# Performance work log

Hardware: AMD Instinct MI355X
Metric: run time of the kernel (lower is better)

The kernel has to match this reference:

```python
import jax, jax.numpy as jnp
import numpy as np


def _maxpool2x2(x):
    # x: [B, C, H, W] -> [B, C, H//2, W//2], 2x2 max pool stride 2
    B, C, H, W = x.shape
    return x.reshape(B, C, H // 2, 2, W // 2, 2).max(axis=(3, 5))


def setup_inputs() -> dict:
    key = jax.random.key(0)
    ks = jax.random.split(key, 5)
    C = 64
    B, H, W = 16, 64, 64
    x = jax.random.normal(ks[0], (B, C, H, W), dtype=jnp.float32)
    s = 0.05
    W_theta = jax.random.normal(ks[1], (C // 8, C), dtype=jnp.float32) * s
    W_phi = jax.random.normal(ks[2], (C // 8, C), dtype=jnp.float32) * s
    W_g = jax.random.normal(ks[3], (C // 2, C), dtype=jnp.float32) * s
    W_attn = jax.random.normal(ks[4], (C, C // 2), dtype=jnp.float32) * s
    sigma = jnp.zeros((1,), dtype=jnp.float32)
    return {"x": x, "W_theta": W_theta, "W_phi": W_phi, "W_g": W_g,
            "W_attn": W_attn, "sigma": sigma}


def reference(x, W_theta, W_phi, W_g, W_attn, sigma):
    B, C, H, W = x.shape
    HW = H * W
    # 1x1 convs are channel GEMMs
    theta = jnp.einsum('oc,bchw->bohw', W_theta, x).reshape(B, C // 8, HW)
    phi = jnp.einsum('oc,bchw->bohw', W_phi, x)
    phi = _maxpool2x2(phi).reshape(B, C // 8, HW // 4)
    # attn: [B, HW, HW//4]
    attn = jax.nn.softmax(jnp.einsum('bcq,bck->bqk', theta, phi), axis=-1)
    g = jnp.einsum('oc,bchw->bohw', W_g, x)
    g = _maxpool2x2(g).reshape(B, C // 2, HW // 4)
    # attn_g: [B, C//2, HW]
    attn_g = jnp.einsum('bck,bqk->bcq', g, attn).reshape(B, C // 2, H, W)
    attn_g = jnp.einsum('oc,bchw->bohw', W_attn, attn_g)
    return x + sigma[0] * attn_g
```

## Files before the change

### kernel.cpp

```cpp
#include <hip/hip_runtime.h>
#include <math.h>

#define B_ 16
#define C_ 64
#define HW_ 4096
#define PHW_ 1024

typedef __attribute__((ext_vector_type(8))) short bf8;
typedef __attribute__((ext_vector_type(16))) float fv16;

union FU { bf8 v; unsigned u[4]; };

__device__ inline unsigned short f2bf(float f) {
    unsigned u = __float_as_uint(f);
    return (unsigned short)((u + 0x7FFFu + ((u >> 16) & 1u)) >> 16);
}
__device__ inline unsigned packbf(float a, float b) {
    return (unsigned)f2bf(a) | ((unsigned)f2bf(b) << 16);
}
__device__ inline unsigned packtr(float a, float b) {
    return (__float_as_uint(a) >> 16) | (__float_as_uint(b) & 0xFFFF0000u);
}

__global__ __launch_bounds__(256) void conv_stage(
    const float* __restrict__ x,
    const float* __restrict__ Wt,
    const float* __restrict__ Wp,
    const float* __restrict__ Wg,
    float* __restrict__ theta,
    unsigned short* __restrict__ phi_pack,
    unsigned short* __restrict__ g_pack)
{
    __shared__ float sx[64][128];
    __shared__ float poolh[2][40][33];

    const int t  = threadIdx.x;
    const int b  = blockIdx.x >> 5;
    const int h2 = blockIdx.x & 31;

    const float* xbase = x + (size_t)b * C_ * HW_ + h2 * 128;
    for (int f = t; f < 2048; f += 256) {
        int c = f >> 5, j4 = f & 31;
        *(float4*)&sx[c][j4 * 4] = *(const float4*)&xbase[(size_t)c * HW_ + j4 * 4];
    }

    const int wv = t >> 6, lane = t & 63, lo = lane & 31, hi = lane >> 5;

    FU wa[2][4];
    {
        const float* r0 = (lo < 8)  ? (Wt + lo * 64)
                        : (lo < 16) ? (Wp + (lo - 8) * 64)
                                    : (Wg + (lo - 16) * 64);
        const float* r1 = Wg + ((lo < 16) ? (16 + lo) : 0) * 64;
#pragma unroll
        for (int cs = 0; cs < 4; cs++) {
            const int c0 = cs * 16 + hi * 8;
            float4 a0 = *(const float4*)&r0[c0];
            float4 b0 = *(const float4*)&r0[c0 + 4];
            wa[0][cs].u[0] = packbf(a0.x, a0.y); wa[0][cs].u[1] = packbf(a0.z, a0.w);
            wa[0][cs].u[2] = packbf(b0.x, b0.y); wa[0][cs].u[3] = packbf(b0.z, b0.w);
            float4 a1 = *(const float4*)&r1[c0];
            float4 b1 = *(const float4*)&r1[c0 + 4];
            if (lo >= 16) { a1 = make_float4(0.f,0.f,0.f,0.f); b1 = make_float4(0.f,0.f,0.f,0.f); }
            wa[1][cs].u[0] = packbf(a1.x, a1.y); wa[1][cs].u[1] = packbf(a1.z, a1.w);
            wa[1][cs].u[2] = packbf(b1.x, b1.y); wa[1][cs].u[3] = packbf(b1.z, b1.w);
        }
    }
    __syncthreads();

    fv16 acc0, acc1;
#pragma unroll
    for (int r = 0; r < 16; r++) { acc0[r] = 0.f; acc1[r] = 0.f; }

    const int px = wv * 32 + lo;
#pragma unroll
    for (int cs = 0; cs < 4; cs++) {
        const float* sp = &sx[cs * 16 + hi * 8][px];
        float v[8];
#pragma unroll
        for (int j = 0; j < 8; j++) v[j] = sp[j * 128];
        FU xb;
        xb.u[0] = packbf(v[0], v[1]); xb.u[1] = packbf(v[2], v[3]);
        xb.u[2] = packbf(v[4], v[5]); xb.u[3] = packbf(v[6], v[7]);
        acc0 = __builtin_amdgcn_mfma_f32_32x32x16_bf16(wa[0][cs].v, xb.v, acc0, 0, 0, 0);
        acc1 = __builtin_amdgcn_mfma_f32_32x32x16_bf16(wa[1][cs].v, xb.v, acc1, 0, 0, 0);
    }

    {
        float* tp = theta + (size_t)b * 8 * HW_ + h2 * 128 + px;
#pragma unroll
        for (int r = 0; r < 4; r++) tp[(size_t)(r + 4 * hi) * HW_] = acc0[r];
    }

    const int prow = wv >> 1;
    const int pcol = (wv & 1) * 16 + (lo >> 1);
#pragma unroll
    for (int r = 4; r < 16; r++) {
        float vv = acc0[r];
        float hm = fmaxf(vv, __shfl_xor(vv, 1));
        if ((lane & 1) == 0) {
            int m = (r & 3) + 8 * (r >> 2) + 4 * hi;
            poolh[prow][m - 8][pcol] = hm;
        }
    }
#pragma unroll
    for (int r = 0; r < 8; r++) {
        float vv = acc1[r];
        float hm = fmaxf(vv, __shfl_xor(vv, 1));
        if ((lane & 1) == 0) {
            int m1 = (r & 3) + 8 * (r >> 2) + 4 * hi;
            poolh[prow][24 + m1][pcol] = hm;
        }
    }
    __syncthreads();

    if (t < 64) {
        unsigned u0 = 0, u1 = 0, u2 = 0, u3 = 0;
        if (t < 32) {
            float v[8];
#pragma unroll
            for (int j = 0; j < 8; j++)
                v[j] = fmaxf(poolh[0][j][t], poolh[1][j][t]);
            u0 = packbf(v[0], v[1]); u1 = packbf(v[2], v[3]);
            u2 = packbf(v[4], v[5]); u3 = packbf(v[6], v[7]);
        }
        uint4 pkt = make_uint4(u0, u1, u2, u3);
        *(uint4*)(phi_pack + ((size_t)((b * 32 + h2) * 64 + t)) * 8) = pkt;
    } else if (t < 192) {
        const int tt  = t - 64;
        const int ktl = tt >> 6;
        const int ln  = tt & 63;
        const int c   = ln & 31;
        const int hh  = ln >> 5;
        float v[8];
#pragma unroll
        for (int j = 0; j < 8; j++) {
            int p = ktl * 16 + hh * 8 + j;
            v[j] = fmaxf(poolh[0][8 + c][p], poolh[1][8 + c][p]);
        }
        uint4 pkt = make_uint4(packbf(v[0], v[1]), packbf(v[2], v[3]),
                               packbf(v[4], v[5]), packbf(v[6], v[7]));
        *(uint4*)(g_pack + ((size_t)((b * 64 + h2 * 2 + ktl) * 64 + ln)) * 8) = pkt;
    }
}

__global__ __launch_bounds__(256, 4) void attn_mfma(
    const float* __restrict__ theta_g,
    const unsigned short* __restrict__ phi_pack,
    const unsigned short* __restrict__ g_pack,
    const float* __restrict__ Wa,
    const float* __restrict__ x,
    const float* __restrict__ sigma,
    float* __restrict__ out)
{
    __shared__ float comb[4][64][17];

    const int t = threadIdx.x, wave = t >> 6, lane = t & 63;
    const int lo = lane & 31, hi = lane >> 5;
    const int qtile = blockIdx.x * 2 + (wave >> 1);
    const int khalf = wave & 1;
    const int b = qtile >> 7, qt = qtile & 127;
    const int qg = qt * 32 + lo;

    FU tb; tb.u[0] = tb.u[1] = tb.u[2] = tb.u[3] = 0;
    if (hi == 0) {
        const float LOG2E = 1.4426950408889634f;
        float tv[8];
#pragma unroll
        for (int j = 0; j < 8; j++)
            tv[j] = theta_g[(((size_t)b * 8 + j) << 12) + qg] * LOG2E;
        tb.u[0] = packbf(tv[0], tv[1]); tb.u[1] = packbf(tv[2], tv[3]);
        tb.u[2] = packbf(tv[4], tv[5]); tb.u[3] = packbf(tv[6], tv[7]);
    }

    fv16 zf, acc;
#pragma unroll
    for (int r = 0; r < 16; r++) { zf[r] = 0.f; acc[r] = 0.f; }
    float ps = 0.f;

    const int kt0 = khalf * 16;
    const unsigned short* phip = phi_pack + ((size_t)((b * 32 + kt0) * 64 + lane)) * 8;
    const unsigned short* gp   = g_pack   + ((size_t)((b * 64 + kt0 * 2) * 64 + lane)) * 8;

#pragma unroll 2
    for (int i = 0; i < 16; i++) {
        FU pa, ga0, ga1;
        pa.v  = *(const bf8*)(phip + (size_t)i * 512);
        ga0.v = *(const bf8*)(gp + (size_t)i * 1024);
        ga1.v = *(const bf8*)(gp + (size_t)i * 1024 + 512);
        fv16 s = __builtin_amdgcn_mfma_f32_32x32x16_bf16(pa.v, tb.v, zf, 0, 0, 0);

        {
            unsigned pk[4], qk[4];
#pragma unroll
            for (int u = 0; u < 4; u++) {
                float p0 = __builtin_amdgcn_exp2f(s[2 * u]);
                float p1 = __builtin_amdgcn_exp2f(s[2 * u + 1]);
                ps += p0 + p1;
                pk[u] = packtr(p0, p1);
            }
#pragma unroll
            for (int u = 0; u < 4; u++) qk[u] = (unsigned)__shfl_xor((int)pk[u], 32);
            FU pb;
            pb.u[0] = hi ? qk[2] : pk[0]; pb.u[1] = hi ? qk[3] : pk[1];
            pb.u[2] = hi ? pk[2] : qk[0]; pb.u[3] = hi ? pk[3] : qk[1];
            acc = __builtin_amdgcn_mfma_f32_32x32x16_bf16(ga0.v, pb.v, acc, 0, 0, 0);
        }
        {
            unsigned pk[4], qk[4];
#pragma unroll
            for (int u = 0; u < 4; u++) {
                float p0 = __builtin_amdgcn_exp2f(s[8 + 2 * u]);
                float p1 = __builtin_amdgcn_exp2f(s[9 + 2 * u]);
                ps += p0 + p1;
                pk[u] = packtr(p0, p1);
            }
#pragma unroll
            for (int u = 0; u < 4; u++) qk[u] = (unsigned)__shfl_xor((int)pk[u], 32);
            FU pb;
            pb.u[0] = hi ? qk[2] : pk[0]; pb.u[1] = hi ? qk[3] : pk[1];
            pb.u[2] = hi ? pk[2] : qk[0]; pb.u[3] = hi ? pk[3] : qk[1];
            acc = __builtin_amdgcn_mfma_f32_32x32x16_bf16(ga1.v, pb.v, acc, 0, 0, 0);
        }
    }

#pragma unroll
    for (int r = 0; r < 16; r++) comb[wave][lane][r] = acc[r];
    comb[wave][lane][16] = ps;
    __syncthreads();
    const int pw = wave ^ 1;
#pragma unroll
    for (int r = 0; r < 16; r++) acc[r] += comb[pw][lane][r];
    ps += comb[pw][lane][16];

    float lsum = ps + __shfl_xor(ps, 32);
    float inv = 1.f / lsum;

    float on[16];
#pragma unroll
    for (int r = 0; r < 16; r++) on[r] = acc[r] * inv;
    unsigned pk[8], qk[8];
#pragma unroll
    for (int i = 0; i < 8; i++) pk[i] = packtr(on[2 * i], on[2 * i + 1]);
#pragma unroll
    for (int i = 0; i < 8; i++) qk[i] = (unsigned)__shfl_xor((int)pk[i], 32);
    FU ob0, ob1;
    ob0.u[0] = hi ? qk[2] : pk[0]; ob0.u[1] = hi ? qk[3] : pk[1];
    ob0.u[2] = hi ? pk[2] : qk[0]; ob0.u[3] = hi ? pk[3] : qk[1];
    ob1.u[0] = hi ? qk[6] : pk[4]; ob1.u[1] = hi ? qk[7] : pk[5];
    ob1.u[2] = hi ? pk[6] : qk[4]; ob1.u[3] = hi ? pk[7] : qk[5];

    FU wa0, wa1;
    {
        const float* wr = Wa + (khalf * 32 + lo) * 32;
#pragma unroll
        for (int ktw = 0; ktw < 2; ktw++) {
            float w8[8];
#pragma unroll
            for (int j = 0; j < 8; j++) w8[j] = wr[ktw * 16 + hi * 8 + j];
            FU f;
            f.u[0] = packbf(w8[0], w8[1]); f.u[1] = packbf(w8[2], w8[3]);
            f.u[2] = packbf(w8[4], w8[5]); f.u[3] = packbf(w8[6], w8[7]);
            if (ktw == 0) wa0 = f; else wa1 = f;
        }
    }
    fv16 d2 = __builtin_amdgcn_mfma_f32_32x32x16_bf16(wa0.v, ob0.v, zf, 0, 0, 0);
    d2 = __builtin_amdgcn_mfma_f32_32x32x16_bf16(wa1.v, ob1.v, d2, 0, 0, 0);

    const float sig = sigma[0];
#pragma unroll
    for (int r = 0; r < 16; r++) {
        int row = (r & 3) + ((r >> 2) << 3) + (hi << 2);
        int o = khalf * 32 + row;
        size_t idx = (((size_t)b * 64 + o) << 12) + qg;
        out[idx] = x[idx] + sig * d2[r];
    }
}

extern "C" void kernel_launch(void* const* d_in, const int* in_sizes, int n_in,
                              void* d_out, int out_size, void* d_ws, size_t ws_size,
                              hipStream_t stream) {
    const float* x     = (const float*)d_in[0];
    const float* Wt    = (const float*)d_in[1];
    const float* Wp    = (const float*)d_in[2];
    const float* Wg    = (const float*)d_in[3];
    const float* Wa    = (const float*)d_in[4];
    const float* sigma = (const float*)d_in[5];
    float* out = (float*)d_out;

    float* theta = (float*)d_ws;
    unsigned short* phi_pack = (unsigned short*)(theta + (size_t)B_ * 8 * HW_);
    unsigned short* g_pack   = phi_pack + (size_t)B_ * 32 * 64 * 8;

    conv_stage<<<512, 256, 0, stream>>>(x, Wt, Wp, Wg, theta, phi_pack, g_pack);
    attn_mfma<<<1024, 256, 0, stream>>>(theta, phi_pack, g_pack, Wa, x, sigma, out);
}
```

Before: 101.0 us.

## Pre-pack theta as bf16 and use permlane32 swaps instead of shuffles

The conv stage now writes theta already scaled by log2e and packed as bf16 in the MFMA operand layout, so the attention kernel loads one 16-byte vector per lane instead of eight strided fp32 loads. The phi pack buffer drops its zero-filled upper half, and only the low lanes load it. The cross-half exchanges before the P·G and output MFMAs use permlane32_swap instead of ds_bpermute-style shuffles with selects. This cuts workspace traffic and LDS-path shuffles, but the permlane swap relies on gfx950-specific semantics and bf16 rounding now happens earlier.

```diff
diff --git a/kernel.cpp b/kernel.cpp
--- a/kernel.cpp
+++ b/kernel.cpp
@@ -20,6 +20,10 @@
 }
 __device__ inline unsigned packtr(float a, float b) {
     return (__float_as_uint(a) >> 16) | (__float_as_uint(b) & 0xFFFF0000u);
+}
+__device__ inline void pl32(unsigned &a, unsigned &b) {
+    auto r = __builtin_amdgcn_permlane32_swap((int)a, (int)b, false, false);
+    a = (unsigned)r[0]; b = (unsigned)r[1];
 }
 
 __global__ __launch_bounds__(256) void conv_stage(
@@ -27,7 +31,7 @@
     const float* __restrict__ Wt,
     const float* __restrict__ Wp,
     const float* __restrict__ Wg,
-    float* __restrict__ theta,
+    unsigned short* __restrict__ theta_pack,
     unsigned short* __restrict__ phi_pack,
     unsigned short* __restrict__ g_pack)
 {
@@ -87,9 +91,11 @@
     }
 
     {
-        float* tp = theta + (size_t)b * 8 * HW_ + h2 * 128 + px;
-#pragma unroll
-        for (int r = 0; r < 4; r++) tp[(size_t)(r + 4 * hi) * HW_] = acc0[r];
+        const float LOG2E = 1.4426950408889634f;
+        unsigned u0 = packbf(acc0[0] * LOG2E, acc0[1] * LOG2E);
+        unsigned u1 = packbf(acc0[2] * LOG2E, acc0[3] * LOG2E);
+        unsigned short* tp = theta_pack + ((size_t)b * HW_ + h2 * 128 + px) * 8 + hi * 4;
+        *(uint2*)tp = make_uint2(u0, u1);
     }
 
     const int prow = wv >> 1;
@@ -115,17 +121,15 @@
     __syncthreads();
 
     if (t < 64) {
-        unsigned u0 = 0, u1 = 0, u2 = 0, u3 = 0;
         if (t < 32) {
             float v[8];
 #pragma unroll
             for (int j = 0; j < 8; j++)
                 v[j] = fmaxf(poolh[0][j][t], poolh[1][j][t]);
-            u0 = packbf(v[0], v[1]); u1 = packbf(v[2], v[3]);
-            u2 = packbf(v[4], v[5]); u3 = packbf(v[6], v[7]);
-        }
-        uint4 pkt = make_uint4(u0, u1, u2, u3);
-        *(uint4*)(phi_pack + ((size_t)((b * 32 + h2) * 64 + t)) * 8) = pkt;
+            uint4 pkt = make_uint4(packbf(v[0], v[1]), packbf(v[2], v[3]),
+                                   packbf(v[4], v[5]), packbf(v[6], v[7]));
+            *(uint4*)(phi_pack + ((size_t)((b * 32 + h2) * 32 + t)) * 8) = pkt;
+        }
     } else if (t < 192) {
         const int tt  = t - 64;
         const int ktl = tt >> 6;
@@ -145,7 +149,7 @@
 }
 
 __global__ __launch_bounds__(256, 4) void attn_mfma(
-    const float* __restrict__ theta_g,
+    const unsigned short* __restrict__ theta_pack,
     const unsigned short* __restrict__ phi_pack,
     const unsigned short* __restrict__ g_pack,
     const float* __restrict__ Wa,
@@ -164,13 +168,8 @@
 
     FU tb; tb.u[0] = tb.u[1] = tb.u[2] = tb.u[3] = 0;
     if (hi == 0) {
-        const float LOG2E = 1.4426950408889634f;
-        float tv[8];
-#pragma unroll
-        for (int j = 0; j < 8; j++)
-            tv[j] = theta_g[(((size_t)b * 8 + j) << 12) + qg] * LOG2E;
-        tb.u[0] = packbf(tv[0], tv[1]); tb.u[1] = packbf(tv[2], tv[3]);
-        tb.u[2] = packbf(tv[4], tv[5]); tb.u[3] = packbf(tv[6], tv[7]);
+        uint4 p = *(const uint4*)(theta_pack + ((size_t)b * HW_ + qg) * 8);
+        tb.u[0] = p.x; tb.u[1] = p.y; tb.u[2] = p.z; tb.u[3] = p.w;
     }
 
     fv16 zf, acc;
@@ -179,47 +178,71 @@
     float ps = 0.f;
 
     const int kt0 = khalf * 16;
-    const unsigned short* phip = phi_pack + ((size_t)((b * 32 + kt0) * 64 + lane)) * 8;
+    const unsigned short* phip = phi_pack + ((size_t)((b * 32 + kt0) * 32 + lo)) * 8;
     const unsigned short* gp   = g_pack   + ((size_t)((b * 64 + kt0 * 2) * 64 + lane)) * 8;
+
+    FU pa; pa.u[0] = pa.u[1] = pa.u[2] = pa.u[3] = 0;
 
 #pragma unroll 2
     for (int i = 0; i < 16; i++) {
-        FU pa, ga0, ga1;
-        pa.v  = *(const bf8*)(phip + (size_t)i * 512);
+        FU ga0, ga1;
+        if (hi == 0) pa.v = *(const bf8*)(phip + (size_t)i * 256);
         ga0.v = *(const bf8*)(gp + (size_t)i * 1024);
         ga1.v = *(const bf8*)(gp + (size_t)i * 1024 + 512);
         fv16 s = __builtin_amdgcn_mfma_f32_32x32x16_bf16(pa.v, tb.v, zf, 0, 0, 0);
 
         {
-            unsigned pk[4], qk[4];
-#pragma unroll
-            for (int u = 0; u < 4; u++) {
-                float p0 = __builtin_amdgcn_exp2f(s[2 * u]);
-                float p1 = __builtin_amdgcn_exp2f(s[2 * u + 1]);
-                ps += p0 + p1;
-                pk[u] = packtr(p0, p1);
-            }
-#pragma unroll
-            for (int u = 0; u < 4; u++) qk[u] = (unsigned)__shfl_xor((int)pk[u], 32);
+            unsigned pk0, pk1, pk2, pk3;
+            {
+                float p0 = __builtin_amdgcn_exp2f(s[0]);
+                float p1 = __builtin_amdgcn_exp2f(s[1]);
+                ps += p0 + p1; pk0 = packtr(p0, p1);
+            }
+            {
+                float p0 = __builtin_amdgcn_exp2f(s[2]);
+                float p1 = __builtin_amdgcn_exp2f(s[3]);
+                ps += p0 + p1; pk1 = packtr(p0, p1);
+            }
+            {
+                float p0 = __builtin_amdgcn_exp2f(s[4]);
+                float p1 = __builtin_amdgcn_exp2f(s[5]);
+                ps += p0 + p1; pk2 = packtr(p0, p1);
+            }
+            {
+                float p0 = __builtin_amdgcn_exp2f(s[6]);
+                float p1 = __builtin_amdgcn_exp2f(s[7]);
+                ps += p0 + p1; pk3 = packtr(p0, p1);
+            }
+            pl32(pk0, pk2); pl32(pk1, pk3);
             FU pb;
-            pb.u[0] = hi ? qk[2] : pk[0]; pb.u[1] = hi ? qk[3] : pk[1];
-            pb.u[2] = hi ? pk[2] : qk[0]; pb.u[3] = hi ? pk[3] : qk[1];
+            pb.u[0] = pk0; pb.u[1] = pk1; pb.u[2] = pk2; pb.u[3] = pk3;
             acc = __builtin_amdgcn_mfma_f32_32x32x16_bf16(ga0.v, pb.v, acc, 0, 0, 0);
         }
         {
-            unsigned pk[4], qk[4];
-#pragma unroll
-            for (int u = 0; u < 4; u++) {
-                float p0 = __builtin_amdgcn_exp2f(s[8 + 2 * u]);
-                float p1 = __builtin_amdgcn_exp2f(s[9 + 2 * u]);
-                ps += p0 + p1;
-                pk[u] = packtr(p0, p1);
-            }
-#pragma unroll
-            for (int u = 0; u < 4; u++) qk[u] = (unsigned)__shfl_xor((int)pk[u], 32);
+            unsigned pk0, pk1, pk2, pk3;
+            {
+                float p0 = __builtin_amdgcn_exp2f(s[8]);
+                float p1 = __builtin_amdgcn_exp2f(s[9]);
+                ps += p0 + p1; pk0 = packtr(p0, p1);
+            }
+            {
+                float p0 = __builtin_amdgcn_exp2f(s[10]);
+                float p1 = __builtin_amdgcn_exp2f(s[11]);
+                ps += p0 + p1; pk1 = packtr(p0, p1);
+            }
+            {
+                float p0 = __builtin_amdgcn_exp2f(s[12]);
+                float p1 = __builtin_amdgcn_exp2f(s[13]);
+                ps += p0 + p1; pk2 = packtr(p0, p1);
+            }
+            {
+                float p0 = __builtin_amdgcn_exp2f(s[14]);
+                float p1 = __builtin_amdgcn_exp2f(s[15]);
+                ps += p0 + p1; pk3 = packtr(p0, p1);
+            }
+            pl32(pk0, pk2); pl32(pk1, pk3);
             FU pb;
-            pb.u[0] = hi ? qk[2] : pk[0]; pb.u[1] = hi ? qk[3] : pk[1];
-            pb.u[2] = hi ? pk[2] : qk[0]; pb.u[3] = hi ? pk[3] : qk[1];
+            pb.u[0] = pk0; pb.u[1] = pk1; pb.u[2] = pk2; pb.u[3] = pk3;
             acc = __builtin_amdgcn_mfma_f32_32x32x16_bf16(ga1.v, pb.v, acc, 0, 0, 0);
         }
     }
@@ -239,16 +262,14 @@
     float on[16];
 #pragma unroll
     for (int r = 0; r < 16; r++) on[r] = acc[r] * inv;
-    unsigned pk[8], qk[8];
+    unsigned pk[8];
 #pragma unroll
     for (int i = 0; i < 8; i++) pk[i] = packtr(on[2 * i], on[2 * i + 1]);
-#pragma unroll
-    for (int i = 0; i < 8; i++) qk[i] = (unsigned)__shfl_xor((int)pk[i], 32);
+    pl32(pk[0], pk[2]); pl32(pk[1], pk[3]);
+    pl32(pk[4], pk[6]); pl32(pk[5], pk[7]);
     FU ob0, ob1;
-    ob0.u[0] = hi ? qk[2] : pk[0]; ob0.u[1] = hi ? qk[3] : pk[1];
-    ob0.u[2] = hi ? pk[2] : qk[0]; ob0.u[3] = hi ? pk[3] : qk[1];
-    ob1.u[0] = hi ? qk[6] : pk[4]; ob1.u[1] = hi ? qk[7] : pk[5];
-    ob1.u[2] = hi ? pk[6] : qk[4]; ob1.u[3] = hi ? pk[7] : qk[5];
+    ob0.u[0] = pk[0]; ob0.u[1] = pk[1]; ob0.u[2] = pk[2]; ob0.u[3] = pk[3];
+    ob1.u[0] = pk[4]; ob1.u[1] = pk[5]; ob1.u[2] = pk[6]; ob1.u[3] = pk[7];
 
     FU wa0, wa1;
     {
@@ -288,10 +309,10 @@
     const float* sigma = (const float*)d_in[5];
     float* out = (float*)d_out;
 
-    float* theta = (float*)d_ws;
-    unsigned short* phi_pack = (unsigned short*)(theta + (size_t)B_ * 8 * HW_);
-    unsigned short* g_pack   = phi_pack + (size_t)B_ * 32 * 64 * 8;
-
-    conv_stage<<<512, 256, 0, stream>>>(x, Wt, Wp, Wg, theta, phi_pack, g_pack);
-    attn_mfma<<<1024, 256, 0, stream>>>(theta, phi_pack, g_pack, Wa, x, sigma, out);
-}
+    unsigned short* theta_pack = (unsigned short*)d_ws;
+    unsigned short* phi_pack   = theta_pack + (size_t)B_ * HW_ * 8;
+    unsigned short* g_pack     = phi_pack + (size_t)B_ * 32 * 32 * 8;
+
+    conv_stage<<<512, 256, 0, stream>>>(x, Wt, Wp, Wg, theta_pack, phi_pack, g_pack);
+    attn_mfma<<<1024, 256, 0, stream>>>(theta_pack, phi_pack, g_pack, Wa, x, sigma, out);
+}
```

Result: no change. 100.4 us (-0.6%).
